# Kernel optimization log

Hardware: AMD Instinct MI355X
Metric: run time of the kernel (lower is better)

The kernel has to match this reference:

```python
import jax, jax.numpy as jnp
import numpy as np

N_NODES = 100000
N_EDGES = 1600000
NODE_DIM = 128
EDGE_DIM = 32
HIDDEN_DIM = 256


def _linear_params(key, fan_in, fan_out):
    kw, kb = jax.random.split(key)
    bound = 1.0 / np.sqrt(fan_in)
    W = jax.random.uniform(kw, (fan_in, fan_out), minval=-bound, maxval=bound, dtype=jnp.float32)
    b = jax.random.uniform(kb, (fan_out,), minval=-bound, maxval=bound, dtype=jnp.float32)
    return W, b


def setup_inputs() -> dict:
    key = jax.random.key(0)
    ks = jax.random.split(key, 8)
    x = jax.random.normal(ks[0], (N_NODES, NODE_DIM), dtype=jnp.float32)
    edge_index = jax.random.randint(ks[1], (2, N_EDGES), 0, N_NODES, dtype=jnp.int64)
    edge_attr = jax.random.normal(ks[2], (N_EDGES, EDGE_DIM), dtype=jnp.float32)
    congestion = jax.random.uniform(ks[3], (N_NODES,), dtype=jnp.float32)
    msg_in = 2 * NODE_DIM + EDGE_DIM + 1
    mW1, mb1 = _linear_params(ks[4], msg_in, HIDDEN_DIM)
    mW2, mb2 = _linear_params(ks[5], HIDDEN_DIM, NODE_DIM)
    uW1, ub1 = _linear_params(ks[6], 2 * NODE_DIM, HIDDEN_DIM)
    uW2, ub2 = _linear_params(ks[7], HIDDEN_DIM, NODE_DIM)
    return {
        "x": x, "edge_index": edge_index, "edge_attr": edge_attr, "congestion": congestion,
        "mW1": mW1, "mb1": mb1, "mW2": mW2, "mb2": mb2,
        "uW1": uW1, "ub1": ub1, "uW2": uW2, "ub2": ub2,
    }


def reference(x, edge_index, edge_attr, congestion, mW1, mb1, mW2, mb2, uW1, ub1, uW2, ub2):
    src, dst = edge_index[0], edge_index[1]
    # gather node features and src congestion, concat along feature dim  [E, 2D+edge_dim+1]
    msg_in = jnp.concatenate(
        [x[src], x[dst], edge_attr, congestion[src][:, None]], axis=-1)
    h = jax.nn.relu(msg_in @ mW1 + mb1)          # [E, hidden]
    messages = h @ mW2 + mb2                     # [E, node_dim]
    # scatter_add messages into destination nodes  [N, node_dim]
    aggregated = jax.ops.segment_sum(messages, dst, num_segments=x.shape[0])
    upd_in = jnp.concatenate([x, aggregated], axis=-1)  # [N, 2*node_dim]
    h2 = jax.nn.relu(upd_in @ uW1 + ub1)
    x_new = h2 @ uW2 + ub2                       # [N, node_dim]
    return x_new
```

## Files before the change

kernel.cpp:

```cpp
#include <hip/hip_runtime.h>

#define E_TOTAL 1600000
#define NN 100000
#define D 128
#define ED 32
#define H 256

typedef __attribute__((ext_vector_type(8))) short s16x8;
typedef __attribute__((ext_vector_type(4))) short s16x4;
typedef __attribute__((ext_vector_type(4))) float f32x4;

#define MFMA(a, b, c) __builtin_amdgcn_mfma_f32_16x16x32_bf16((a), (b), (c), 0, 0, 0)

__device__ __forceinline__ short f2bf(float f) {
    unsigned u = __builtin_bit_cast(unsigned, f);
    u += 0x7fffu + ((u >> 16) & 1u);
    return (short)(u >> 16);
}

__device__ __forceinline__ void gll16(const void* g, void* l) {
    __builtin_amdgcn_global_load_lds(
        (const __attribute__((address_space(1))) void*)g,
        (__attribute__((address_space(3))) void*)l, 16, 0, 0);
}

__global__ void k_cvt_x(const float* __restrict__ x, short* __restrict__ xb, int n) {
    int i = (blockIdx.x * blockDim.x + threadIdx.x) * 4;
    if (i >= n) return;
    f32x4 v = *(const f32x4*)(x + i);
    s16x4 o;
    o[0] = f2bf(v[0]); o[1] = f2bf(v[1]); o[2] = f2bf(v[2]); o[3] = f2bf(v[3]);
    *(s16x4*)(xb + i) = o;
}

__global__ void k_swz(const float* __restrict__ W, short* __restrict__ out,
                      int K, int N, int total) {
    int idx = blockIdx.x * blockDim.x + threadIdx.x;
    if (idx >= total) return;
    int j    = idx & 7;
    int lane = (idx >> 3) & 63;
    int rest = idx >> 9;
    int NT   = N >> 4;
    int nt   = rest % NT;
    int t    = rest / NT;
    int k    = t * 32 + (lane >> 4) * 8 + j;
    int col  = nt * 16 + (lane & 15);
    float v  = (k < K) ? W[k * N + col] : 0.f;
    out[idx] = f2bf(v);
}

__global__ void k_hist(const int* __restrict__ ei, int* __restrict__ cnt) {
    int e = blockIdx.x * blockDim.x + threadIdx.x;
    if (e >= E_TOTAL) return;
    atomicAdd(&cnt[ei[E_TOTAL + e]], 1);
}

__global__ void k_scan1(int* __restrict__ cnt, int* __restrict__ psum, int n) {
    __shared__ int wsum[16];
    __shared__ int woff[16];
    const int tid = threadIdx.x, lane = tid & 63, wv = tid >> 6;
    int i = blockIdx.x * 1024 + tid;
    int v = (i < n) ? cnt[i] : 0;
    int s = v;
#pragma unroll
    for (int off = 1; off < 64; off <<= 1) {
        int u = __shfl_up(s, off, 64);
        if (lane >= off) s += u;
    }
    if (lane == 63) wsum[wv] = s;
    __syncthreads();
    if (wv == 0 && lane < 16) {
        int t = wsum[lane];
        int sc = t;
#pragma unroll
        for (int off = 1; off < 16; off <<= 1) {
            int u = __shfl_up(sc, off, 16);
            if (lane >= off) sc += u;
        }
        woff[lane] = sc - t;
    }
    __syncthreads();
    int excl = (s - v) + woff[wv];
    if (i < n) cnt[i] = excl;
    if (tid == 1023) psum[blockIdx.x] = excl + v;
}

__global__ void k_scan2(int* __restrict__ psum, int nb) {
    __shared__ int w0;
    const int tid = threadIdx.x, lane = tid & 63, wv = tid >> 6;
    int v = (tid < nb) ? psum[tid] : 0;
    int s = v;
#pragma unroll
    for (int off = 1; off < 64; off <<= 1) {
        int u = __shfl_up(s, off, 64);
        if (lane >= off) s += u;
    }
    if (wv == 0 && lane == 63) w0 = s;
    __syncthreads();
    int excl = (s - v) + (wv ? w0 : 0);
    if (tid < nb) psum[tid] = excl;
}

__global__ void k_scan3(const int* __restrict__ psum, int* __restrict__ cnt, int n) {
    int i = blockIdx.x * 1024 + threadIdx.x;
    if (i < n) cnt[i] += psum[blockIdx.x];
}

__global__ void k_perm(const int* __restrict__ ei, int* __restrict__ cursor,
                       int* __restrict__ perm, int2* __restrict__ srcdst) {
    int e = blockIdx.x * blockDim.x + threadIdx.x;
    if (e >= E_TOTAL) return;
    int s = ei[e], d = ei[E_TOTAL + e];
    int pos = atomicAdd(&cursor[d], 1);
    perm[pos] = e;
    srcdst[pos] = make_int2(s, d);
}

__global__ __launch_bounds__(512, 4)
void k_edge(const short* __restrict__ xb, const int* __restrict__ perm,
            const int2* __restrict__ srcdst,
            const float* __restrict__ eattr, const float* __restrict__ cong,
            const short* __restrict__ W1s, const float* __restrict__ b1,
            const short* __restrict__ W2s, const float* __restrict__ b2,
            float* __restrict__ agg) {
    __shared__ char smem[73728];
    __shared__ int   dst_s[128];
    __shared__ short cong_s[128];

    const int tid  = threadIdx.x;
    const int lane = tid & 63;
    const int w    = tid >> 6;
    const int m    = lane & 15;
    const int q    = lane >> 4;
    const int p0b  = blockIdx.x * 128;

    {
        int edge = w * 16 + (lane >> 2);
        int2 sd  = srcdst[p0b + edge];
        int kqs  = (lane & 3) ^ ((lane >> 4) & 3);
        const char* gx0 = (const char*)xb + (long)sd.x * 256 + kqs * 16;
        const char* gx1 = (const char*)xb + (long)sd.y * 256 + kqs * 16;
#pragma unroll
        for (int t = 0; t < 4; t++)
            gll16(gx0 + t * 64, smem + t * 8192 + w * 1024);
#pragma unroll
        for (int t = 0; t < 4; t++)
            gll16(gx1 + t * 64, smem + (4 + t) * 8192 + w * 1024);
        int ea = perm[p0b + edge];
        const float* ge = eattr + (long)ea * ED + kqs * 8;
        f32x4 e0 = *(const f32x4*)ge, e1 = *(const f32x4*)(ge + 4);
        s16x8 ev;
#pragma unroll
        for (int j = 0; j < 4; j++) { ev[j] = f2bf(e0[j]); ev[4 + j] = f2bf(e1[j]); }
        *(s16x8*)(smem + 8 * 8192 + w * 1024 + lane * 16) = ev;
        if (tid < 128) {
            int2 sd2 = srcdst[p0b + tid];
            dst_s[tid]  = sd2.y;
            cong_s[tid] = f2bf(cong[sd2.x]);
        }
    }
    __syncthreads();

    const int rdoff = m * 64 + ((q ^ ((m >> 2) & 3)) << 4);

    f32x4 acc[8][2];
#pragma unroll
    for (int mt = 0; mt < 8; mt++) {
        acc[mt][0] = (f32x4){0.f, 0.f, 0.f, 0.f};
        acc[mt][1] = (f32x4){0.f, 0.f, 0.f, 0.f};
    }
#pragma unroll
    for (int t = 0; t < 9; t++) {
        const short* bw = W1s + (t * 16 + w * 2) * 512 + lane * 8;
        s16x8 b0 = *(const s16x8*)bw;
        s16x8 b1v = *(const s16x8*)(bw + 512);
#pragma unroll
        for (int mt = 0; mt < 8; mt++) {
            s16x8 a = *(const s16x8*)(smem + t * 8192 + mt * 1024 + rdoff);
            acc[mt][0] = MFMA(a, b0, acc[mt][0]);
            acc[mt][1] = MFMA(a, b1v, acc[mt][1]);
        }
    }
    {
        const short* bw = W1s + (9 * 16 + w * 2) * 512 + lane * 8;
        s16x8 b0 = *(const s16x8*)bw;
        s16x8 b1v = *(const s16x8*)(bw + 512);
#pragma unroll
        for (int mt = 0; mt < 8; mt++) {
            s16x8 a = (s16x8){0, 0, 0, 0, 0, 0, 0, 0};
            short cv = cong_s[mt * 16 + m];
            a[0] = (q == 0) ? cv : (short)0;
            acc[mt][0] = MFMA(a, b0, acc[mt][0]);
            acc[mt][1] = MFMA(a, b1v, acc[mt][1]);
        }
    }
    __syncthreads();

    {
        float bb0 = b1[w * 32 + m];
        float bb1 = b1[w * 32 + 16 + m];
        short* hbase = (short*)(smem + w * 8192);
        const int so0 = ((((m >> 3) + 0)) ^ q) * 8 + (m & 7);
        const int so1 = ((((m >> 3) + 2)) ^ q) * 8 + (m & 7);
#pragma unroll
        for (int mt = 0; mt < 8; mt++) {
#pragma unroll
            for (int r = 0; r < 4; r++) {
                int edge = mt * 16 + q * 4 + r;
                float v0 = acc[mt][0][r] + bb0;
                float v1 = acc[mt][1][r] + bb1;
                hbase[edge * 32 + so0] = f2bf(v0 > 0.f ? v0 : 0.f);
                hbase[edge * 32 + so1] = f2bf(v1 > 0.f ? v1 : 0.f);
            }
        }
    }
    __syncthreads();

    f32x4 acc2[8];
#pragma unroll
    for (int mt = 0; mt < 8; mt++) acc2[mt] = (f32x4){0.f, 0.f, 0.f, 0.f};
#pragma unroll
    for (int t2 = 0; t2 < 8; t2++) {
        s16x8 b = *(const s16x8*)(W2s + (t2 * 8 + w) * 512 + lane * 8);
#pragma unroll
        for (int mt = 0; mt < 8; mt++) {
            s16x8 a = *(const s16x8*)(smem + t2 * 8192 + mt * 1024 + rdoff);
            acc2[mt] = MFMA(a, b, acc2[mt]);
        }
    }
    __syncthreads();

    {
        float (*mbuf)[132] = (float (*)[132])smem;
        float bb = b2[w * 16 + m];
#pragma unroll
        for (int mt = 0; mt < 8; mt++)
#pragma unroll
            for (int r = 0; r < 4; r++)
                mbuf[mt * 16 + q * 4 + r][w * 16 + m] = acc2[mt][r] + bb;
    }
    __syncthreads();

    {
        float (*mbuf)[132] = (float (*)[132])smem;
        const int qtr = tid >> 7, cc = tid & 127;
        float s = 0.f;
        int prev = dst_s[qtr * 32];
        for (int row = qtr * 32; row < qtr * 32 + 32; row++) {
            int dcur = dst_s[row];
            if (dcur != prev) {
                __hip_atomic_fetch_add(agg + (long)prev * D + cc, s,
                                       __ATOMIC_RELAXED, __HIP_MEMORY_SCOPE_AGENT);
                s = 0.f; prev = dcur;
            }
            s += mbuf[row][cc];
        }
        __hip_atomic_fetch_add(agg + (long)prev * D + cc, s,
                               __ATOMIC_RELAXED, __HIP_MEMORY_SCOPE_AGENT);
    }
}

__global__ __launch_bounds__(512, 4)
void k_node(const short* __restrict__ xb, const float* __restrict__ agg,
            const short* __restrict__ U1s, const float* __restrict__ b1,
            const short* __restrict__ U2s, const float* __restrict__ b2,
            float* __restrict__ out) {
    __shared__ char smem[65536];
    const int tid  = threadIdx.x;
    const int lane = tid & 63;
    const int w    = tid >> 6;
    const int m    = lane & 15;
    const int q    = lane >> 4;
    const int r0   = blockIdx.x * 128;

    {
        int rowl = w * 16 + (lane >> 2);
        int grow = r0 + rowl;
        int gc   = grow < NN ? grow : 0;
        int kqs  = (lane & 3) ^ ((lane >> 4) & 3);
        const char* gx = (const char*)xb + (long)gc * 256 + kqs * 16;
#pragma unroll
        for (int t = 0; t < 4; t++)
            gll16(gx + t * 64, smem + t * 8192 + w * 1024);
        const float* ga = agg + (long)gc * D + kqs * 8;
#pragma unroll
        for (int t = 0; t < 4; t++) {
            f32x4 a0 = *(const f32x4*)(ga + t * 32);
            f32x4 a1 = *(const f32x4*)(ga + t * 32 + 4);
            s16x8 v;
#pragma unroll
            for (int j = 0; j < 4; j++) { v[j] = f2bf(a0[j]); v[4 + j] = f2bf(a1[j]); }
            *(s16x8*)(smem + (4 + t) * 8192 + w * 1024 + lane * 16) = v;
        }
    }
    __syncthreads();

    const int rdoff = m * 64 + ((q ^ ((m >> 2) & 3)) << 4);

    f32x4 acc[8][2];
#pragma unroll
    for (int mt = 0; mt < 8; mt++) {
        acc[mt][0] = (f32x4){0.f, 0.f, 0.f, 0.f};
        acc[mt][1] = (f32x4){0.f, 0.f, 0.f, 0.f};
    }
#pragma unroll
    for (int t = 0; t < 8; t++) {
        const short* bw = U1s + (t * 16 + w * 2) * 512 + lane * 8;
        s16x8 b0 = *(const s16x8*)bw;
        s16x8 b1v = *(const s16x8*)(bw + 512);
#pragma unroll
        for (int mt = 0; mt < 8; mt++) {
            s16x8 a = *(const s16x8*)(smem + t * 8192 + mt * 1024 + rdoff);
            acc[mt][0] = MFMA(a, b0, acc[mt][0]);
            acc[mt][1] = MFMA(a, b1v, acc[mt][1]);
        }
    }
    __syncthreads();

    {
        float bb0 = b1[w * 32 + m];
        float bb1 = b1[w * 32 + 16 + m];
        short* hbase = (short*)(smem + w * 8192);
        const int so0 = ((((m >> 3) + 0)) ^ q) * 8 + (m & 7);
        const int so1 = ((((m >> 3) + 2)) ^ q) * 8 + (m & 7);
#pragma unroll
        for (int mt = 0; mt < 8; mt++) {
#pragma unroll
            for (int r = 0; r < 4; r++) {
                int row = mt * 16 + q * 4 + r;
                float v0 = acc[mt][0][r] + bb0;
                float v1 = acc[mt][1][r] + bb1;
                hbase[row * 32 + so0] = f2bf(v0 > 0.f ? v0 : 0.f);
                hbase[row * 32 + so1] = f2bf(v1 > 0.f ? v1 : 0.f);
            }
        }
    }
    __syncthreads();

    f32x4 acc2[8];
#pragma unroll
    for (int mt = 0; mt < 8; mt++) acc2[mt] = (f32x4){0.f, 0.f, 0.f, 0.f};
#pragma unroll
    for (int t2 = 0; t2 < 8; t2++) {
        s16x8 b = *(const s16x8*)(U2s + (t2 * 8 + w) * 512 + lane * 8);
#pragma unroll
        for (int mt = 0; mt < 8; mt++) {
            s16x8 a = *(const s16x8*)(smem + t2 * 8192 + mt * 1024 + rdoff);
            acc2[mt] = MFMA(a, b, acc2[mt]);
        }
    }

    {
        float bb = b2[w * 16 + m];
#pragma unroll
        for (int mt = 0; mt < 8; mt++)
#pragma unroll
            for (int r = 0; r < 4; r++) {
                int grow = r0 + mt * 16 + q * 4 + r;
                if (grow < NN)
                    out[(long)grow * D + w * 16 + m] = acc2[mt][r] + bb;
            }
    }
}

extern "C" void kernel_launch(void* const* d_in, const int* in_sizes, int n_in,
                              void* d_out, int out_size, void* d_ws, size_t ws_size,
                              hipStream_t stream) {
    const float* x     = (const float*)d_in[0];
    const int*   ei    = (const int*)d_in[1];
    const float* eattr = (const float*)d_in[2];
    const float* cong  = (const float*)d_in[3];
    const float* mW1   = (const float*)d_in[4];
    const float* mb1   = (const float*)d_in[5];
    const float* mW2   = (const float*)d_in[6];
    const float* mb2   = (const float*)d_in[7];
    const float* uW1   = (const float*)d_in[8];
    const float* ub1   = (const float*)d_in[9];
    const float* uW2   = (const float*)d_in[10];
    const float* ub2   = (const float*)d_in[11];

    char* ws = (char*)d_ws;
    float* agg    = (float*)ws;
    short* xb     = (short*)(ws + 51200000);
    short* W1s    = (short*)(ws + 76800000);
    short* W2s    = (short*)(ws + 76963840);
    short* U1s    = (short*)(ws + 77029376);
    short* U2s    = (short*)(ws + 77160448);
    int*   cnt    = (int*)(ws + 77225984);
    int*   perm   = (int*)(ws + 77625984);
    int2*  srcdst = (int2*)(ws + 84025984);
    int*   psum   = (int*)(ws + 96825984);

    hipMemsetAsync(agg, 0, (size_t)NN * D * sizeof(float), stream);
    hipMemsetAsync(cnt, 0, (size_t)NN * sizeof(int), stream);

    k_cvt_x<<<(NN * D / 4 + 255) / 256, 256, 0, stream>>>(x, xb, NN * D);

    int tW1 = 10 * 16 * 512, tW2 = 8 * 8 * 512, tU1 = 8 * 16 * 512, tU2 = 8 * 8 * 512;
    k_swz<<<(tW1 + 255) / 256, 256, 0, stream>>>(mW1, W1s, 289, 256, tW1);
    k_swz<<<(tW2 + 255) / 256, 256, 0, stream>>>(mW2, W2s, 256, 128, tW2);
    k_swz<<<(tU1 + 255) / 256, 256, 0, stream>>>(uW1, U1s, 256, 256, tU1);
    k_swz<<<(tU2 + 255) / 256, 256, 0, stream>>>(uW2, U2s, 256, 128, tU2);

    int nb = (NN + 1023) / 1024;
    k_hist<<<(E_TOTAL + 255) / 256, 256, 0, stream>>>(ei, cnt);
    k_scan1<<<nb, 1024, 0, stream>>>(cnt, psum, NN);
    k_scan2<<<1, 128, 0, stream>>>(psum, nb);
    k_scan3<<<nb, 1024, 0, stream>>>(psum, cnt, NN);
    k_perm<<<(E_TOTAL + 255) / 256, 256, 0, stream>>>(ei, cnt, perm, srcdst);

    k_edge<<<E_TOTAL / 128, 512, 0, stream>>>(xb, perm, srcdst, eattr, cong,
                                              W1s, mb1, W2s, mb2, agg);
    k_node<<<(NN + 127) / 128, 512, 0, stream>>>(xb, agg, U1s, ub1, U2s, ub2,
                                                 (float*)d_out);
}
```

Baseline: 959.1 us.

## Halve block size to 4 waves, each computing wider N-tiles per wave

Both the edge and node MLP kernels move from 8 waves of 512 threads to 4 waves of 256 threads per 128-row block. Each wave now computes 64 hidden columns in layer 1 and 32 output columns in layer 2, doubling accumulator registers. Staging loops, the hidden-activation layout and the segmented reduction are adjusted to match. The aim is to reuse each LDS A-fragment load across more MFMAs and cut LDS traffic per flop. The cost is higher register pressure and fewer waves to hide gather latency.

```diff
diff --git a/kernel.cpp b/kernel.cpp
--- a/kernel.cpp
+++ b/kernel.cpp
@@ -116,7 +116,7 @@
     srcdst[pos] = make_int2(s, d);
 }
 
-__global__ __launch_bounds__(512, 4)
+__global__ __launch_bounds__(256, 2)
 void k_edge(const short* __restrict__ xb, const int* __restrict__ perm,
             const int2* __restrict__ srcdst,
             const float* __restrict__ eattr, const float* __restrict__ cong,
@@ -135,24 +135,28 @@
     const int p0b  = blockIdx.x * 128;
 
     {
-        int edge = w * 16 + (lane >> 2);
-        int2 sd  = srcdst[p0b + edge];
-        int kqs  = (lane & 3) ^ ((lane >> 4) & 3);
-        const char* gx0 = (const char*)xb + (long)sd.x * 256 + kqs * 16;
-        const char* gx1 = (const char*)xb + (long)sd.y * 256 + kqs * 16;
-#pragma unroll
-        for (int t = 0; t < 4; t++)
-            gll16(gx0 + t * 64, smem + t * 8192 + w * 1024);
-#pragma unroll
-        for (int t = 0; t < 4; t++)
-            gll16(gx1 + t * 64, smem + (4 + t) * 8192 + w * 1024);
-        int ea = perm[p0b + edge];
-        const float* ge = eattr + (long)ea * ED + kqs * 8;
-        f32x4 e0 = *(const f32x4*)ge, e1 = *(const f32x4*)(ge + 4);
-        s16x8 ev;
-#pragma unroll
-        for (int j = 0; j < 4; j++) { ev[j] = f2bf(e0[j]); ev[4 + j] = f2bf(e1[j]); }
-        *(s16x8*)(smem + 8 * 8192 + w * 1024 + lane * 16) = ev;
+        const int kqs = (lane & 3) ^ ((lane >> 4) & 3);
+#pragma unroll
+        for (int j = 0; j < 2; j++) {
+            int el  = w * 32 + j * 16 + (lane >> 2);
+            int2 sd = srcdst[p0b + el];
+            int  ea = perm[p0b + el];
+            char* dst = smem + (w * 2 + j) * 1024;
+            const char* gx0 = (const char*)xb + (long)sd.x * 256 + kqs * 16;
+            const char* gx1 = (const char*)xb + (long)sd.y * 256 + kqs * 16;
+#pragma unroll
+            for (int t = 0; t < 4; t++)
+                gll16(gx0 + t * 64, dst + t * 8192);
+#pragma unroll
+            for (int t = 0; t < 4; t++)
+                gll16(gx1 + t * 64, dst + (4 + t) * 8192);
+            const float* ge = eattr + (long)ea * ED + kqs * 8;
+            f32x4 e0 = *(const f32x4*)ge, e1 = *(const f32x4*)(ge + 4);
+            s16x8 ev;
+#pragma unroll
+            for (int jj = 0; jj < 4; jj++) { ev[jj] = f2bf(e0[jj]); ev[4 + jj] = f2bf(e1[jj]); }
+            *(s16x8*)(dst + 8 * 8192 + lane * 16) = ev;
+        }
         if (tid < 128) {
             int2 sd2 = srcdst[p0b + tid];
             dst_s[tid]  = sd2.y;
@@ -163,90 +167,101 @@
 
     const int rdoff = m * 64 + ((q ^ ((m >> 2) & 3)) << 4);
 
-    f32x4 acc[8][2];
-#pragma unroll
-    for (int mt = 0; mt < 8; mt++) {
-        acc[mt][0] = (f32x4){0.f, 0.f, 0.f, 0.f};
-        acc[mt][1] = (f32x4){0.f, 0.f, 0.f, 0.f};
-    }
+    f32x4 acc[8][4];
+#pragma unroll
+    for (int mt = 0; mt < 8; mt++)
+#pragma unroll
+        for (int n = 0; n < 4; n++) acc[mt][n] = (f32x4){0.f, 0.f, 0.f, 0.f};
+
 #pragma unroll
     for (int t = 0; t < 9; t++) {
-        const short* bw = W1s + (t * 16 + w * 2) * 512 + lane * 8;
-        s16x8 b0 = *(const s16x8*)bw;
-        s16x8 b1v = *(const s16x8*)(bw + 512);
+        s16x8 b[4];
+        const short* bw = W1s + (t * 16 + w * 4) * 512 + lane * 8;
+#pragma unroll
+        for (int n = 0; n < 4; n++) b[n] = *(const s16x8*)(bw + n * 512);
 #pragma unroll
         for (int mt = 0; mt < 8; mt++) {
             s16x8 a = *(const s16x8*)(smem + t * 8192 + mt * 1024 + rdoff);
-            acc[mt][0] = MFMA(a, b0, acc[mt][0]);
-            acc[mt][1] = MFMA(a, b1v, acc[mt][1]);
-        }
-    }
-    {
-        const short* bw = W1s + (9 * 16 + w * 2) * 512 + lane * 8;
-        s16x8 b0 = *(const s16x8*)bw;
-        s16x8 b1v = *(const s16x8*)(bw + 512);
+#pragma unroll
+            for (int n = 0; n < 4; n++) acc[mt][n] = MFMA(a, b[n], acc[mt][n]);
+        }
+    }
+    {
+        s16x8 b[4];
+        const short* bw = W1s + (9 * 16 + w * 4) * 512 + lane * 8;
+#pragma unroll
+        for (int n = 0; n < 4; n++) b[n] = *(const s16x8*)(bw + n * 512);
 #pragma unroll
         for (int mt = 0; mt < 8; mt++) {
             s16x8 a = (s16x8){0, 0, 0, 0, 0, 0, 0, 0};
             short cv = cong_s[mt * 16 + m];
             a[0] = (q == 0) ? cv : (short)0;
-            acc[mt][0] = MFMA(a, b0, acc[mt][0]);
-            acc[mt][1] = MFMA(a, b1v, acc[mt][1]);
-        }
-    }
-    __syncthreads();
-
-    {
-        float bb0 = b1[w * 32 + m];
-        float bb1 = b1[w * 32 + 16 + m];
-        short* hbase = (short*)(smem + w * 8192);
-        const int so0 = ((((m >> 3) + 0)) ^ q) * 8 + (m & 7);
-        const int so1 = ((((m >> 3) + 2)) ^ q) * 8 + (m & 7);
-#pragma unroll
-        for (int mt = 0; mt < 8; mt++) {
-#pragma unroll
-            for (int r = 0; r < 4; r++) {
-                int edge = mt * 16 + q * 4 + r;
-                float v0 = acc[mt][0][r] + bb0;
-                float v1 = acc[mt][1][r] + bb1;
-                hbase[edge * 32 + so0] = f2bf(v0 > 0.f ? v0 : 0.f);
-                hbase[edge * 32 + so1] = f2bf(v1 > 0.f ? v1 : 0.f);
-            }
-        }
-    }
-    __syncthreads();
-
-    f32x4 acc2[8];
-#pragma unroll
-    for (int mt = 0; mt < 8; mt++) acc2[mt] = (f32x4){0.f, 0.f, 0.f, 0.f};
+#pragma unroll
+            for (int n = 0; n < 4; n++) acc[mt][n] = MFMA(a, b[n], acc[mt][n]);
+        }
+    }
+    __syncthreads();
+
+    {
+        short* hb = (short*)smem;
+#pragma unroll
+        for (int n = 0; n < 4; n++) {
+            const int chunk = 2 * w + (n >> 1);
+            const int srq   = (n & 1) * 2 + (m >> 3);
+            const int phys  = srq ^ q;
+            const float bias = b1[w * 64 + n * 16 + m];
+            const int base = chunk * 4096 + (q * 4) * 32 + phys * 8 + (m & 7);
+#pragma unroll
+            for (int mt = 0; mt < 8; mt++) {
+#pragma unroll
+                for (int r = 0; r < 4; r++) {
+                    float v = acc[mt][n][r] + bias;
+                    hb[base + mt * 512 + r * 32] = f2bf(v > 0.f ? v : 0.f);
+                }
+            }
+        }
+    }
+    __syncthreads();
+
+    f32x4 acc2[8][2];
+#pragma unroll
+    for (int mt = 0; mt < 8; mt++) {
+        acc2[mt][0] = (f32x4){0.f, 0.f, 0.f, 0.f};
+        acc2[mt][1] = (f32x4){0.f, 0.f, 0.f, 0.f};
+    }
 #pragma unroll
     for (int t2 = 0; t2 < 8; t2++) {
-        s16x8 b = *(const s16x8*)(W2s + (t2 * 8 + w) * 512 + lane * 8);
+        s16x8 b0  = *(const s16x8*)(W2s + (t2 * 8 + w * 2) * 512 + lane * 8);
+        s16x8 b1v = *(const s16x8*)(W2s + (t2 * 8 + w * 2 + 1) * 512 + lane * 8);
 #pragma unroll
         for (int mt = 0; mt < 8; mt++) {
             s16x8 a = *(const s16x8*)(smem + t2 * 8192 + mt * 1024 + rdoff);
-            acc2[mt] = MFMA(a, b, acc2[mt]);
+            acc2[mt][0] = MFMA(a, b0, acc2[mt][0]);
+            acc2[mt][1] = MFMA(a, b1v, acc2[mt][1]);
         }
     }
     __syncthreads();
 
     {
         float (*mbuf)[132] = (float (*)[132])smem;
-        float bb = b2[w * 16 + m];
+        float bb0 = b2[w * 32 + m];
+        float bb1 = b2[w * 32 + 16 + m];
 #pragma unroll
         for (int mt = 0; mt < 8; mt++)
 #pragma unroll
-            for (int r = 0; r < 4; r++)
-                mbuf[mt * 16 + q * 4 + r][w * 16 + m] = acc2[mt][r] + bb;
+            for (int r = 0; r < 4; r++) {
+                mbuf[mt * 16 + q * 4 + r][w * 32 + m]      = acc2[mt][0][r] + bb0;
+                mbuf[mt * 16 + q * 4 + r][w * 32 + 16 + m] = acc2[mt][1][r] + bb1;
+            }
     }
     __syncthreads();
 
     {
         float (*mbuf)[132] = (float (*)[132])smem;
-        const int qtr = tid >> 7, cc = tid & 127;
+        const int half = tid >> 7, cc = tid & 127;
         float s = 0.f;
-        int prev = dst_s[qtr * 32];
-        for (int row = qtr * 32; row < qtr * 32 + 32; row++) {
+        int prev = dst_s[half * 64];
+        for (int row = half * 64; row < half * 64 + 64; row++) {
             int dcur = dst_s[row];
             if (dcur != prev) {
                 __hip_atomic_fetch_add(agg + (long)prev * D + cc, s,
@@ -260,7 +275,7 @@
     }
 }
 
-__global__ __launch_bounds__(512, 4)
+__global__ __launch_bounds__(256, 2)
 void k_node(const short* __restrict__ xb, const float* __restrict__ agg,
             const short* __restrict__ U1s, const float* __restrict__ b1,
             const short* __restrict__ U2s, const float* __restrict__ b2,
@@ -274,91 +289,105 @@
     const int r0   = blockIdx.x * 128;
 
     {
-        int rowl = w * 16 + (lane >> 2);
-        int grow = r0 + rowl;
-        int gc   = grow < NN ? grow : 0;
-        int kqs  = (lane & 3) ^ ((lane >> 4) & 3);
-        const char* gx = (const char*)xb + (long)gc * 256 + kqs * 16;
-#pragma unroll
-        for (int t = 0; t < 4; t++)
-            gll16(gx + t * 64, smem + t * 8192 + w * 1024);
-        const float* ga = agg + (long)gc * D + kqs * 8;
-#pragma unroll
-        for (int t = 0; t < 4; t++) {
-            f32x4 a0 = *(const f32x4*)(ga + t * 32);
-            f32x4 a1 = *(const f32x4*)(ga + t * 32 + 4);
-            s16x8 v;
-#pragma unroll
-            for (int j = 0; j < 4; j++) { v[j] = f2bf(a0[j]); v[4 + j] = f2bf(a1[j]); }
-            *(s16x8*)(smem + (4 + t) * 8192 + w * 1024 + lane * 16) = v;
+        const int kqs = (lane & 3) ^ ((lane >> 4) & 3);
+#pragma unroll
+        for (int j = 0; j < 2; j++) {
+            int rowl = w * 32 + j * 16 + (lane >> 2);
+            int grow = r0 + rowl;
+            int gc   = grow < NN ? grow : 0;
+            char* dst = smem + (w * 2 + j) * 1024;
+            const char* gx = (const char*)xb + (long)gc * 256 + kqs * 16;
+#pragma unroll
+            for (int t = 0; t < 4; t++)
+                gll16(gx + t * 64, dst + t * 8192);
+            const float* ga = agg + (long)gc * D + kqs * 8;
+#pragma unroll
+            for (int t = 0; t < 4; t++) {
+                f32x4 a0 = *(const f32x4*)(ga + t * 32);
+                f32x4 a1 = *(const f32x4*)(ga + t * 32 + 4);
+                s16x8 v;
+#pragma unroll
+                for (int jj = 0; jj < 4; jj++) { v[jj] = f2bf(a0[jj]); v[4 + jj] = f2bf(a1[jj]); }
+                *(s16x8*)(dst + (4 + t) * 8192 + lane * 16) = v;
+            }
         }
     }
     __syncthreads();
 
     const int rdoff = m * 64 + ((q ^ ((m >> 2) & 3)) << 4);
 
-    f32x4 acc[8][2];
-#pragma unroll
-    for (int mt = 0; mt < 8; mt++) {
-        acc[mt][0] = (f32x4){0.f, 0.f, 0.f, 0.f};
-        acc[mt][1] = (f32x4){0.f, 0.f, 0.f, 0.f};
-    }
+    f32x4 acc[8][4];
+#pragma unroll
+    for (int mt = 0; mt < 8; mt++)
+#pragma unroll
+        for (int n = 0; n < 4; n++) acc[mt][n] = (f32x4){0.f, 0.f, 0.f, 0.f};
+
 #pragma unroll
     for (int t = 0; t < 8; t++) {
-        const short* bw = U1s + (t * 16 + w * 2) * 512 + lane * 8;
-        s16x8 b0 = *(const s16x8*)bw;
-        s16x8 b1v = *(const s16x8*)(bw + 512);
+        s16x8 b[4];
+        const short* bw = U1s + (t * 16 + w * 4) * 512 + lane * 8;
+#pragma unroll
+        for (int n = 0; n < 4; n++) b[n] = *(const s16x8*)(bw + n * 512);
 #pragma unroll
         for (int mt = 0; mt < 8; mt++) {
             s16x8 a = *(const s16x8*)(smem + t * 8192 + mt * 1024 + rdoff);
-            acc[mt][0] = MFMA(a, b0, acc[mt][0]);
-            acc[mt][1] = MFMA(a, b1v, acc[mt][1]);
-        }
-    }
-    __syncthreads();
-
-    {
-        float bb0 = b1[w * 32 + m];
-        float bb1 = b1[w * 32 + 16 + m];
-        short* hbase = (short*)(smem + w * 8192);
-        const int so0 = ((((m >> 3) + 0)) ^ q) * 8 + (m & 7);
-        const int so1 = ((((m >> 3) + 2)) ^ q) * 8 + (m & 7);
-#pragma unroll
-        for (int mt = 0; mt < 8; mt++) {
-#pragma unroll
-            for (int r = 0; r < 4; r++) {
-                int row = mt * 16 + q * 4 + r;
-                float v0 = acc[mt][0][r] + bb0;
-                float v1 = acc[mt][1][r] + bb1;
-                hbase[row * 32 + so0] = f2bf(v0 > 0.f ? v0 : 0.f);
-                hbase[row * 32 + so1] = f2bf(v1 > 0.f ? v1 : 0.f);
-            }
-        }
-    }
-    __syncthreads();
-
-    f32x4 acc2[8];
-#pragma unroll
-    for (int mt = 0; mt < 8; mt++) acc2[mt] = (f32x4){0.f, 0.f, 0.f, 0.f};
+#pragma unroll
+            for (int n = 0; n < 4; n++) acc[mt][n] = MFMA(a, b[n], acc[mt][n]);
+        }
+    }
+    __syncthreads();
+
+    {
+        short* hb = (short*)smem;
+#pragma unroll
+        for (int n = 0; n < 4; n++) {
+            const int chunk = 2 * w + (n >> 1);
+            const int srq   = (n & 1) * 2 + (m >> 3);
+            const int phys  = srq ^ q;
+            const float bias = b1[w * 64 + n * 16 + m];
+            const int base = chunk * 4096 + (q * 4) * 32 + phys * 8 + (m & 7);
+#pragma unroll
+            for (int mt = 0; mt < 8; mt++) {
+#pragma unroll
+                for (int r = 0; r < 4; r++) {
+                    float v = acc[mt][n][r] + bias;
+                    hb[base + mt * 512 + r * 32] = f2bf(v > 0.f ? v : 0.f);
+                }
+            }
+        }
+    }
+    __syncthreads();
+
+    f32x4 acc2[8][2];
+#pragma unroll
+    for (int mt = 0; mt < 8; mt++) {
+        acc2[mt][0] = (f32x4){0.f, 0.f, 0.f, 0.f};
+        acc2[mt][1] = (f32x4){0.f, 0.f, 0.f, 0.f};
+    }
 #pragma unroll
     for (int t2 = 0; t2 < 8; t2++) {
-        s16x8 b = *(const s16x8*)(U2s + (t2 * 8 + w) * 512 + lane * 8);
+        s16x8 b0  = *(const s16x8*)(U2s + (t2 * 8 + w * 2) * 512 + lane * 8);
+        s16x8 b1v = *(const s16x8*)(U2s + (t2 * 8 + w * 2 + 1) * 512 + lane * 8);
 #pragma unroll
         for (int mt = 0; mt < 8; mt++) {
             s16x8 a = *(const s16x8*)(smem + t2 * 8192 + mt * 1024 + rdoff);
-            acc2[mt] = MFMA(a, b, acc2[mt]);
-        }
-    }
-
-    {
-        float bb = b2[w * 16 + m];
+            acc2[mt][0] = MFMA(a, b0, acc2[mt][0]);
+            acc2[mt][1] = MFMA(a, b1v, acc2[mt][1]);
+        }
+    }
+
+    {
+        float bb0 = b2[w * 32 + m];
+        float bb1 = b2[w * 32 + 16 + m];
 #pragma unroll
         for (int mt = 0; mt < 8; mt++)
 #pragma unroll
             for (int r = 0; r < 4; r++) {
                 int grow = r0 + mt * 16 + q * 4 + r;
-                if (grow < NN)
-                    out[(long)grow * D + w * 16 + m] = acc2[mt][r] + bb;
+                if (grow < NN) {
+                    out[(long)grow * D + w * 32 + m]      = acc2[mt][0][r] + bb0;
+                    out[(long)grow * D + w * 32 + 16 + m] = acc2[mt][1][r] + bb1;
+                }
             }
     }
 }
@@ -409,8 +438,8 @@
     k_scan3<<<nb, 1024, 0, stream>>>(psum, cnt, NN);
     k_perm<<<(E_TOTAL + 255) / 256, 256, 0, stream>>>(ei, cnt, perm, srcdst);
 
-    k_edge<<<E_TOTAL / 128, 512, 0, stream>>>(xb, perm, srcdst, eattr, cong,
+    k_edge<<<E_TOTAL / 128, 256, 0, stream>>>(xb, perm, srcdst, eattr, cong,
                                               W1s, mb1, W2s, mb2, agg);
-    k_node<<<(NN + 127) / 128, 512, 0, stream>>>(xb, agg, U1s, ub1, U2s, ub2,
+    k_node<<<(NN + 127) / 128, 256, 0, stream>>>(xb, agg, U1s, ub1, U2s, ub2,
                                                  (float*)d_out);
 }
```

New measurement: 1.055 ms. 10.0% more time.
